# Optimization experiments

Hardware: AMD Instinct MI355X
Metric: run time of the kernel (lower is better)

## Reference

```python
import jax, jax.numpy as jnp
import numpy as np

B, S, D, H = 4, 1024, 1024, 16
DK = D // H
N_REL = 5


def setup_inputs() -> dict:
    key = jax.random.key(0)
    ks = jax.random.split(key, 16)
    p = lambda k, shape: (jax.random.normal(k, shape, dtype=jnp.float32) * 0.02)
    return {
        "x": jax.random.normal(ks[0], (B, S, D), dtype=jnp.float32),
        "relation_matrix": jax.random.randint(ks[1], (S, S), 0, N_REL, dtype=jnp.int32),
        "mask": jax.random.randint(ks[2], (B, 1, S, S), 0, 2, dtype=jnp.int32),
        "Wq": p(ks[3], (D, D)), "bq": p(ks[4], (D,)),
        "Wk": p(ks[5], (D, D)), "bk": p(ks[6], (D,)),
        "Wv": p(ks[7], (D, D)), "bv": p(ks[8], (D,)),
        "Wo": p(ks[9], (D, D)), "bo": p(ks[10], (D,)),
        "rel_table": p(ks[11], (N_REL, DK)),
        "gamma": jnp.ones((D,), dtype=jnp.float32),
        "beta": jnp.zeros((D,), dtype=jnp.float32),
    }


def reference(x, relation_matrix, mask, Wq, bq, Wk, bk, Wv, bv, Wo, bo, rel_table, gamma, beta):
    b, s = x.shape[0], x.shape[1]
    residual = x
    # projections -> [B, H, S, DK]
    def proj(W, bias):
        return (x @ W + bias).reshape(b, s, H, DK).transpose(0, 2, 1, 3)
    Q, K, V = proj(Wq, bq), proj(Wk, bk), proj(Wv, bv)
    scores = jnp.einsum('bhid,bhjd->bhij', Q, K) / jnp.sqrt(jnp.float32(DK))
    # relation-embedding additive bias: gather [S,S,DK] then contract with Q
    rel_emb = rel_table[relation_matrix]               # [S, S, DK]
    rel_scores = jnp.einsum('bhid,ijd->bhij', Q, rel_emb)
    scores = scores + rel_scores * 0.5
    scores = jnp.where(mask == 0, jnp.float32(-1e9), scores)
    attention = jax.nn.softmax(scores, axis=-1)
    context = jnp.einsum('bhij,bhjd->bhid', attention, V)
    context = context.transpose(0, 2, 1, 3).reshape(b, s, D)
    output = context @ Wo + bo
    # layer norm (eps = 1e-5, torch default)
    y = output + residual
    mu = jnp.mean(y, axis=-1, keepdims=True)
    var = jnp.mean(jnp.square(y - mu), axis=-1, keepdims=True)
    return (y - mu) * jax.lax.rsqrt(var + 1e-5) * gamma + beta
```

## Files before the change

### kernel.cpp

```cpp
#include <hip/hip_runtime.h>
#include <hip/hip_bf16.h>

typedef unsigned short u16;
typedef unsigned int u32;
typedef unsigned char u8;
typedef __attribute__((ext_vector_type(8))) short short8;
typedef __attribute__((ext_vector_type(4))) float f32x4;

__device__ __forceinline__ float b2f(u16 u) {
    union { float f; u32 i; } z; z.i = ((u32)u) << 16; return z.f;
}
__device__ __forceinline__ u16 f2b(float f) {
    union { float f; u32 i; } z; z.f = f;
    u32 i = z.i;
    u32 r = (i + 0x7FFFu + ((i >> 16) & 1u)) >> 16;
    return (u16)r;
}
__device__ __forceinline__ float ldf(const void* p, size_t i, int f) {
    return f ? ((const float*)p)[i] : b2f(((const u16*)p)[i]);
}
__device__ __forceinline__ void gload_lds16(const void* g, void* l) {
    __builtin_amdgcn_global_load_lds(
        (const __attribute__((address_space(1))) u32*)g,
        (__attribute__((address_space(3))) u32*)l,
        16, 0, 0);
}

struct P14 { const void* p[14]; };
struct S14 { int s[14]; };

__global__ __launch_bounds__(256) void classify_stats(P14 ptrs, S14 szs, int* stats)
{
    __shared__ int   wsm[4], wzr[4], wag[4], way[4], wjk[4];
    __shared__ float wme[4], wmo[4];
    int i = blockIdx.x;
    int t = threadIdx.x, lane = t & 63, w = t >> 6;
    const u16* p16 = (const u16*)ptrs.p[i];
    const u32* p32 = (const u32*)ptrs.p[i];
    int n = szs.s[i];
    int n16 = n < 4096 ? n : 4096;
    int n32 = n16 >> 1;
    int small = 1, zero = 1, allg = 1, anyg = 0, junk = 0;
    float maxe = 0.f, maxo = 0.f;
    for (int k = t; k < n32; k += 256) if (p32[k] >= 8u) small = 0;
    for (int k = t; k < n16; k += 256) {
        u16 ww = p16[k];
        if (ww != 0) zero = 0;
        if (ww == 0x3F80u) anyg = 1;
        else if (ww != 0) allg = 0;
        float a = fabsf(b2f(ww));
        if (k & 1) { if (a < 1e30f && a > maxo) maxo = a; }
        else { if (!(a < 100.0f)) junk++; else if (a > maxe) maxe = a; }
    }
#pragma unroll
    for (int s = 1; s < 64; s <<= 1) {
        small &= __shfl_xor(small, s);
        zero  &= __shfl_xor(zero, s);
        allg  &= __shfl_xor(allg, s);
        anyg  |= __shfl_xor(anyg, s);
        junk  += __shfl_xor(junk, s);
        maxe   = fmaxf(maxe, __shfl_xor(maxe, s));
        maxo   = fmaxf(maxo, __shfl_xor(maxo, s));
    }
    if (lane == 0) { wsm[w]=small; wzr[w]=zero; wag[w]=allg; way[w]=anyg; wjk[w]=junk; wme[w]=maxe; wmo[w]=maxo; }
    __syncthreads();
    if (t == 0) {
        int sm=1,zr=1,ag=1,ay=0,jk=0; float me=0.f,mo=0.f;
        for (int q=0;q<4;++q){ sm&=wsm[q]; zr&=wzr[q]; ag&=wag[q]; ay|=way[q]; jk+=wjk[q]; me=fmaxf(me,wme[q]); mo=fmaxf(mo,wmo[q]); }
        stats[i*8+0]=sm; stats[i*8+1]=zr; stats[i*8+2]=(ag&&ay)?1:0; stats[i*8+3]=jk;
        stats[i*8+4]=__float_as_int(me); stats[i*8+5]=__float_as_int(mo);
    }
}

__global__ __launch_bounds__(64) void classify_bind(S14 szs, const int* stats, int* cls)
{
    if (threadIdx.x != 0) return;
    int xi = -1, mi = -1, ri = -1, rt = -1, gi = -1, bi = -1;
    int wv[4] = {-1,-1,-1,-1}; int nw = 0;
    int bs[4] = {-1,-1,-1,-1}; int nb = 0;
    for (int i = 0; i < 14; ++i) {
        int s = szs.s[i];
        int sm = stats[i*8+0], zr = stats[i*8+1];
        if (s == 4194304) { if (sm) mi = i; else xi = i; }
        else if (s == 1048576) { if (sm) ri = i; else if (nw < 4) wv[nw++] = i; }
        else if (s == 320) rt = i;
        else if (s == 1024) {
            if (zr) bi = i;
            else if (stats[i*8+2]) gi = i;
            else if (nb < 4) bs[nb++] = i;
        }
    }
    bool ok = (xi >= 0) && (mi >= 0) && (ri >= 0) && (rt >= 0) && (gi >= 0) && (bi >= 0)
           && (nw == 4) && (nb == 4);
    if (ok) {
        cls[0] = xi; cls[1] = ri; cls[2] = mi;
        cls[3] = wv[0]; cls[5] = wv[1]; cls[7] = wv[2]; cls[9] = wv[3];
        cls[4] = bs[0]; cls[6] = bs[1]; cls[8] = bs[2]; cls[10] = bs[3];
        cls[11] = rt; cls[12] = gi; cls[13] = bi;
    } else {
        for (int r = 0; r < 14; ++r) cls[r] = r;
    }
    const int froles[12] = {0,3,4,5,6,7,8,9,10,11,12,13};
    for (int r = 0; r < 12; ++r) {
        int role = froles[r]; int idx = cls[role];
        float me = __int_as_float(stats[idx*8+4]);
        float mo = __int_as_float(stats[idx*8+5]);
        cls[16 + role] = (stats[idx*8+3] > 0) || (me == 0.f && mo > 0.f);
    }
    cls[30] = ok ? 1 : 0;
}

__global__ __launch_bounds__(256) void cvt_x_flex(P14 ptrs, const int* cls, u16* xb) {
    const void* x = ptrs.p[cls[0]];
    int f = cls[16];
    int idx = (blockIdx.x * 256 + threadIdx.x) << 2;
    union { u16 u[4]; uint2 v2; } o;
    if (f) {
        float4 v = *(const float4*)((const float*)x + idx);
        o.u[0] = f2b(v.x); o.u[1] = f2b(v.y); o.u[2] = f2b(v.z); o.u[3] = f2b(v.w);
    } else {
        o.v2 = *(const uint2*)((const u16*)x + idx);
    }
    *(uint2*)&xb[idx] = o.v2;
}

__global__ __launch_bounds__(256) void transposeW_flex(P14 ptrs, const int* cls,
                                                       u16* WT3, u16* WoT)
{
    int z = blockIdx.z;
    const void* W = ptrs.p[cls[3 + 2 * z]];
    int f = cls[16 + 3 + 2 * z];
    u16* WT = (z < 3) ? (WT3 + ((size_t)z << 20)) : WoT;
    __shared__ u16 tile[64][72];
    int t = threadIdx.x;
    int n0 = blockIdx.x << 6, k0 = blockIdx.y << 6;
    int r = t >> 2, c = (t & 3) << 4;
    size_t base = (size_t)(k0 + r) * 1024 + n0 + c;
    if (f) {
        const float* src = (const float*)W + base;
#pragma unroll
        for (int x = 0; x < 16; ++x) tile[r][c + x] = f2b(src[x]);
    } else {
        const u16* src = (const u16*)W + base;
#pragma unroll
        for (int x = 0; x < 16; ++x) tile[r][c + x] = src[x];
    }
    __syncthreads();
    union { u16 u[16]; uint4 v[2]; } tmp;
#pragma unroll
    for (int x = 0; x < 16; ++x) tmp.u[x] = tile[c + x][r];
    *(uint4*)&WT[(size_t)(n0 + r) * 1024 + k0 + c]     = tmp.v[0];
    *(uint4*)&WT[(size_t)(n0 + r) * 1024 + k0 + c + 8] = tmp.v[1];
}

__global__ __launch_bounds__(256) void qrel_k(
    const u16* __restrict__ Q, P14 ptrs, const int* cls, float* __restrict__ Qrel)
{
    __shared__ float rt[5][64];
    const void* rel_table = ptrs.p[cls[11]];
    int f9 = cls[16 + 11];
    int t = threadIdx.x;
    for (int p = t; p < 320; p += 256) ((float*)rt)[p] = ldf(rel_table, p, f9);
    __syncthreads();
    int row = blockIdx.x * 256 + t;
    const u16* qrow = Q + ((size_t)row << 6);
    float a0=0.f, a1=0.f, a2=0.f, a3=0.f, a4=0.f;
#pragma unroll
    for (int k8 = 0; k8 < 64; k8 += 8) {
        union { uint4 v; u16 u[8]; } qq;
        qq.v = *(const uint4*)(qrow + k8);
#pragma unroll
        for (int e = 0; e < 8; ++e) {
            float qv = b2f(qq.u[e]);
            a0 += qv * rt[0][k8 + e];
            a1 += qv * rt[1][k8 + e];
            a2 += qv * rt[2][k8 + e];
            a3 += qv * rt[3][k8 + e];
            a4 += qv * rt[4][k8 + e];
        }
    }
    const float S = 0.5f * 1.44269504f;
    float4 o0 = {a0 * S, a1 * S, a2 * S, a3 * S};
    float4 o1 = {a4 * S, -1e9f, -1e9f, -1e9f};
    *(float4*)&Qrel[(size_t)row * 8]     = o0;
    *(float4*)&Qrel[(size_t)row * 8 + 4] = o1;
}

__global__ __launch_bounds__(256) void gemm128_qkv(
    const u16* __restrict__ X, const u16* __restrict__ WT3,
    P14 ptrs, const int* cls,
    u16* __restrict__ Qb, u16* __restrict__ Kb, u16* __restrict__ VTb)
{
    int o = (blockIdx.x & 7) * 192 + (blockIdx.x >> 3);
    int mt = o / 48, rem = o % 48;
    int z = rem >> 4, nt = rem & 15;
    int m0 = mt << 7, n0 = nt << 6;
    const u16* WT = WT3 + ((size_t)z << 20);
    const void* biasp = ptrs.p[cls[4 + 2 * z]];
    int fb = cls[16 + 4 + 2 * z];
    __shared__ u16 As[2][128][4][8];
    __shared__ u16 Bs[2][64][4][8];
    int t = threadIdx.x, lane = t & 63, w = t >> 6;
    int m = lane & 15, quad = lane >> 4;
    int wm = (w >> 1) << 6, wn = (w & 1) << 5;
    int r1 = t >> 2, r2 = 64 + r1, k4 = t & 3;
    const u16* xa  = &X [(size_t)(m0 + r1) * 1024 + k4 * 8];
    const u16* xa2 = &X [(size_t)(m0 + r2) * 1024 + k4 * 8];
    const u16* wb  = &WT[(size_t)(n0 + r1) * 1024 + k4 * 8];
    f32x4 acc[4][2];
#pragma unroll
    for (int i = 0; i < 4; ++i)
#pragma unroll
        for (int j = 0; j < 2; ++j) acc[i][j] = (f32x4){0.f,0.f,0.f,0.f};

    auto stage = [&](int buf, int k0) {
        gload_lds16(xa  + k0, &As[buf][r1][k4][0]);
        gload_lds16(xa2 + k0, &As[buf][r2][k4][0]);
        gload_lds16(wb  + k0, &Bs[buf][r1][k4][0]);
    };
    stage(0, 0);
    __syncthreads();
    int cur = 0;
    for (int k0 = 0; k0 < 1024; k0 += 32) {
        if (k0 + 32 < 1024) stage(cur ^ 1, k0 + 32);
        short8 af[4], bf[2];
#pragma unroll
        for (int mb = 0; mb < 4; ++mb) af[mb] = *(const short8*)&As[cur][wm + mb*16 + m][quad][0];
#pragma unroll
        for (int nb = 0; nb < 2; ++nb) bf[nb] = *(const short8*)&Bs[cur][wn + nb*16 + m][quad][0];
#pragma unroll
        for (int mb = 0; mb < 4; ++mb)
#pragma unroll
            for (int nb = 0; nb < 2; ++nb)
                acc[mb][nb] = __builtin_amdgcn_mfma_f32_16x16x32_bf16(af[mb], bf[nb], acc[mb][nb], 0, 0, 0);
        __syncthreads();
        cur ^= 1;
    }
    if (z == 2) {
#pragma unroll
        for (int nb = 0; nb < 2; ++nb) {
            int gn = n0 + wn + nb*16 + m;
            int h = gn >> 6, dk = gn & 63;
            float bv = ldf(biasp, gn, fb);
            int sx = (dk & 7) << 3;
#pragma unroll
            for (int mb = 0; mb < 4; ++mb) {
                int gmBase = m0 + wm + mb*16 + (quad << 2);
                int bI = gmBase >> 10, sB = gmBase & 1023;
                int pos = (sB & ~63) | ((sB & 63) ^ sx);
                union { u16 u[4]; uint2 v; } o4;
#pragma unroll
                for (int r = 0; r < 4; ++r) o4.u[r] = f2b(acc[mb][nb][r] + bv);
                *(uint2*)&VTb[((size_t)(bI * 16 + h) << 16) + dk * 1024 + pos] = o4.v;
            }
        }
    } else {
        u16* outp = (z == 0) ? Qb : Kb;
#pragma unroll
        for (int nb = 0; nb < 2; ++nb) {
            int gn = n0 + wn + nb*16 + m;
            int h = gn >> 6, dk = gn & 63;
            float bv = ldf(biasp, gn, fb);
#pragma unroll
            for (int mb = 0; mb < 4; ++mb)
#pragma unroll
                for (int r = 0; r < 4; ++r) {
                    int gm = m0 + wm + mb*16 + (quad << 2) + r;
                    int bI = gm >> 10, s = gm & 1023;
                    int dk2 = (z == 1) ? (dk ^ (((quad * 4 + r) & 7) << 3)) : dk;
                    outp[((size_t)((bI * 16 + h) << 10) + s) * 64 + dk2] = f2b(acc[mb][nb][r] + bv);
                }
        }
    }
}

__global__ __launch_bounds__(256) void gemm_out64(
    const u16* __restrict__ A, const u16* __restrict__ WT,
    P14 ptrs, const int* cls, float* __restrict__ y)
{
    const void* bo   = ptrs.p[cls[10]];
    const void* Xres = ptrs.p[cls[0]];
    int f8 = cls[16 + 10], f0 = cls[16];
    int o = (blockIdx.x & 7) * 128 + (blockIdx.x >> 3);
    int nt = o & 15, mt = o >> 4;
    int n0 = nt << 6, m0 = mt << 6;
    __shared__ u16 As[2][64][4][8];
    __shared__ u16 Bs[2][64][4][8];
    int t = threadIdx.x, lane = t & 63, w = t >> 6;
    int m = lane & 15, quad = lane >> 4;
    int wm = (w >> 1) << 5, wn = (w & 1) << 5;
    int r1 = t >> 2, k4 = t & 3;
    const u16* xa  = &A [(size_t)(m0 + r1) * 1024 + k4 * 8];
    const u16* wb  = &WT[(size_t)(n0 + r1) * 1024 + k4 * 8];
    f32x4 acc[2][2];
#pragma unroll
    for (int i = 0; i < 2; ++i)
#pragma unroll
        for (int j = 0; j < 2; ++j) acc[i][j] = (f32x4){0.f,0.f,0.f,0.f};

    auto stage = [&](int buf, int k0) {
        gload_lds16(xa + k0, &As[buf][r1][k4][0]);
        gload_lds16(wb + k0, &Bs[buf][r1][k4][0]);
    };
    stage(0, 0);
    __syncthreads();
    int cur = 0;
    for (int k0 = 0; k0 < 1024; k0 += 32) {
        if (k0 + 32 < 1024) stage(cur ^ 1, k0 + 32);
        short8 af[2], bf[2];
#pragma unroll
        for (int mb = 0; mb < 2; ++mb) af[mb] = *(const short8*)&As[cur][wm + mb*16 + m][quad][0];
#pragma unroll
        for (int nb = 0; nb < 2; ++nb) bf[nb] = *(const short8*)&Bs[cur][wn + nb*16 + m][quad][0];
#pragma unroll
        for (int mb = 0; mb < 2; ++mb)
#pragma unroll
            for (int nb = 0; nb < 2; ++nb)
                acc[mb][nb] = __builtin_amdgcn_mfma_f32_16x16x32_bf16(af[mb], bf[nb], acc[mb][nb], 0, 0, 0);
        __syncthreads();
        cur ^= 1;
    }
#pragma unroll
    for (int nb = 0; nb < 2; ++nb) {
        int gn = n0 + wn + nb*16 + m;
        float bb = ldf(bo, gn, f8);
#pragma unroll
        for (int mb = 0; mb < 2; ++mb)
#pragma unroll
            for (int r = 0; r < 4; ++r) {
                int gm = m0 + wm + mb*16 + (quad << 2) + r;
                size_t idx = (size_t)gm * 1024 + gn;
                y[idx] = acc[mb][nb][r] + bb + ldf(Xres, idx, f0);
            }
    }
}

__global__ __launch_bounds__(256) void make_codes(P14 ptrs, const int* cls, u8* codes)
{
    const int* relmat = (const int*)ptrs.p[cls[1]];
    const int* maskp  = (const int*)ptrs.p[cls[2]];
    int bid = blockIdx.x;
    int b = bid >> 8, ti = (bid >> 4) & 15, tj = bid & 15;
    int t = threadIdx.x, lane = t & 63, w = t >> 6;
    int m = lane & 15, quad = lane >> 4;
    const int* mb = maskp + ((size_t)b << 20);
    union { uint4 v; u8 c[16]; } out;
#pragma unroll
    for (int jb = 0; jb < 4; ++jb) {
        int j = tj * 64 + jb * 16 + m;
#pragma unroll
        for (int r = 0; r < 4; ++r) {
            int i = ti * 64 + w * 16 + (quad << 2) + r;
            size_t off = (size_t)i * 1024 + j;
            out.c[jb * 4 + r] = mb[off] ? (u8)relmat[off] : (u8)5;
        }
    }
    ((uint4*)codes)[(size_t)bid * 256 + t] = out.v;
}

__global__ __launch_bounds__(256) void attn_mfma(
    const u16* __restrict__ Q, const u16* __restrict__ K, const u16* __restrict__ VT,
    const float* __restrict__ Qrel, const u8* __restrict__ codes, u16* __restrict__ ctx)
{
    int raw = blockIdx.x;
    int bid = (raw & 7) * 128 + (raw >> 3);
    int bh = bid >> 4, ti = bid & 15;
    int i0 = ti << 6;
    int b = bh >> 4, h = bh & 15;
    const u16* Qp = Q  + ((size_t)bh << 16);
    const u16* Kp = K  + ((size_t)bh << 16);
    const u16* Vp = VT + ((size_t)bh << 16);
    const uint4* ctile = (const uint4*)codes + ((size_t)((b * 16 + ti) * 16) << 8);

    __shared__ u16 Ks[2][64][64];
    __shared__ u16 Vt[64][64];
    __shared__ u16 Pls[64][72];
    __shared__ float Qrl[64][9];

    int t = threadIdx.x, lane = t & 63, w = t >> 6;
    int m = lane & 15, quad = lane >> 4;

    {
        float2 qv = *(const float2*)&Qrel[(((size_t)bh << 10) + i0) * 8 + (t << 1)];
        Qrl[t >> 2][(t & 3) << 1]       = qv.x;
        Qrl[t >> 2][((t & 3) << 1) + 1] = qv.y;
    }

    short8 qfrag0, qfrag1;
    {
        const u16* qr = Qp + (size_t)(i0 + w * 16 + m) * 64 + quad * 8;
        qfrag0 = *(const short8*)qr;
        qfrag1 = *(const short8*)(qr + 32);
    }
    f32x4 O[4];
    float l_part[4];
#pragma unroll
    for (int d = 0; d < 4; ++d) O[d] = (f32x4){0.f,0.f,0.f,0.f};
#pragma unroll
    for (int r = 0; r < 4; ++r) l_part[r] = 0.f;

    int srow = t >> 3, scol8 = (t & 7) << 3;
    const u16* ks0 = Kp + (size_t)srow * 64 + scol8;
    const u16* ks1 = ks0 + 32 * 64;
    const u16* vs0 = Vp + (size_t)srow * 1024 + scol8;
    const u16* vs1 = vs0 + 32 * 1024;

    auto stageK = [&](int buf, int j0) {
        gload_lds16(ks0 + (size_t)j0 * 64, &Ks[buf][srow][scol8]);
        gload_lds16(ks1 + (size_t)j0 * 64, &Ks[buf][srow + 32][scol8]);
    };
    auto stageV = [&](int j0) {
        gload_lds16(vs0 + j0, &Vt[srow][scol8]);
        gload_lds16(vs1 + j0, &Vt[srow + 32][scol8]);
    };

    const float SC = 0.125f * 1.44269504f;
    int kx = (m & 7) << 3;

    stageK(0, 0);
    stageV(0);
    uint4 cN = ctile[t];
    __syncthreads();
    int cur = 0;

    for (int j0 = 0; j0 < 1024; j0 += 64) {
        bool next = (j0 + 64 < 1024);
        if (next) stageK(cur ^ 1, j0 + 64);

        f32x4 acc[4];
#pragma unroll
        for (int jb = 0; jb < 4; ++jb) {
            acc[jb] = (f32x4){0.f,0.f,0.f,0.f};
            short8 kb0 = *(const short8*)&Ks[cur][jb * 16 + m][(quad * 8) ^ kx];
            short8 kb1 = *(const short8*)&Ks[cur][jb * 16 + m][(32 + quad * 8) ^ kx];
            acc[jb] = __builtin_amdgcn_mfma_f32_16x16x32_bf16(qfrag0, kb0, acc[jb], 0, 0, 0);
            acc[jb] = __builtin_amdgcn_mfma_f32_16x16x32_bf16(qfrag1, kb1, acc[jb], 0, 0, 0);
        }
        union { uint4 v; u8 c[16]; } cd;
        cd.v = cN;
        if (next) cN = ctile[(((j0 + 64) >> 6) << 8) + t];

        float sc[4][4];
#pragma unroll
        for (int jb = 0; jb < 4; ++jb) {
#pragma unroll
            for (int r = 0; r < 4; ++r) {
                int il = w * 16 + (quad << 2) + r;
                float p = exp2f(acc[jb][r] * SC + Qrl[il][cd.c[jb * 4 + r]]);
                sc[jb][r] = p;
                l_part[r] += p;
            }
        }
#pragma unroll
        for (int jb = 0; jb < 4; ++jb)
#pragma unroll
            for (int r = 0; r < 4; ++r)
                Pls[w * 16 + (quad << 2) + r][jb * 16 + m] = f2b(sc[jb][r]);

        __syncthreads();

        short8 pa0 = *(const short8*)&Pls[w * 16 + m][quad * 8];
        short8 pa1 = *(const short8*)&Pls[w * 16 + m][quad * 8 + 32];
#pragma unroll
        for (int db = 0; db < 4; ++db) {
            short8 vb0 = *(const short8*)&Vt[db * 16 + m][(quad * 8) ^ kx];
            short8 vb1 = *(const short8*)&Vt[db * 16 + m][(32 + quad * 8) ^ kx];
            O[db] = __builtin_amdgcn_mfma_f32_16x16x32_bf16(pa0, vb0, O[db], 0, 0, 0);
            O[db] = __builtin_amdgcn_mfma_f32_16x16x32_bf16(pa1, vb1, O[db], 0, 0, 0);
        }

        __syncthreads();
        if (next) stageV(j0 + 64);
        cur ^= 1;
    }
    float linv[4];
#pragma unroll
    for (int r = 0; r < 4; ++r) {
        float l = l_part[r];
        l += __shfl_xor(l, 1);
        l += __shfl_xor(l, 2);
        l += __shfl_xor(l, 4);
        l += __shfl_xor(l, 8);
        linv[r] = 1.0f / fmaxf(l, 1e-35f);
    }
#pragma unroll
    for (int db = 0; db < 4; ++db)
#pragma unroll
        for (int r = 0; r < 4; ++r) {
            int il = w * 16 + (quad << 2) + r;
            size_t addr = ((size_t)(b * 1024 + i0 + il)) * 1024 + h * 64 + db * 16 + m;
            ctx[addr] = f2b(O[db][r] * linv[r]);
        }
}

__global__ __launch_bounds__(256) void ln_k(
    float* __restrict__ y, P14 ptrs, const int* cls)
{
    const void* gamma = ptrs.p[cls[12]];
    const void* beta  = ptrs.p[cls[13]];
    int f10 = cls[16 + 12], f11 = cls[16 + 13];
    int row = blockIdx.x, t = threadIdx.x;
    float4 v = *(const float4*)&y[(size_t)row * 1024 + (t << 2)];
    float s = v.x + v.y + v.z + v.w;
#pragma unroll
    for (int mm = 1; mm < 64; mm <<= 1) s += __shfl_xor(s, mm);
    __shared__ float sm[8];
    int w = t >> 6, lane = t & 63;
    if (lane == 0) sm[w] = s;
    __syncthreads();
    float mu = (sm[0] + sm[1] + sm[2] + sm[3]) * (1.0f / 1024.0f);
    float dx = v.x - mu, dy = v.y - mu, dz = v.z - mu, dw = v.w - mu;
    float q = dx * dx + dy * dy + dz * dz + dw * dw;
#pragma unroll
    for (int mm = 1; mm < 64; mm <<= 1) q += __shfl_xor(q, mm);
    if (lane == 0) sm[4 + w] = q;
    __syncthreads();
    float var = (sm[4] + sm[5] + sm[6] + sm[7]) * (1.0f / 1024.0f);
    float rs = rsqrtf(var + 1e-5f);
    int c = t << 2;
    float4 o;
    o.x = dx * rs * ldf(gamma, c,     f10) + ldf(beta, c,     f11);
    o.y = dy * rs * ldf(gamma, c + 1, f10) + ldf(beta, c + 1, f11);
    o.z = dz * rs * ldf(gamma, c + 2, f10) + ldf(beta, c + 2, f11);
    o.w = dw * rs * ldf(gamma, c + 3, f10) + ldf(beta, c + 3, f11);
    *(float4*)&y[(size_t)row * 1024 + c] = o;
}

extern "C" void kernel_launch(void* const* d_in, const int* in_sizes, int n_in,
                              void* d_out, int out_size, void* d_ws, size_t ws_size,
                              hipStream_t stream) {
    (void)out_size; (void)ws_size;
    P14 ptrs; S14 szs;
    for (int i = 0; i < 14; ++i) {
        ptrs.p[i] = (i < n_in) ? d_in[i] : d_in[0];
        szs.s[i]  = (i < n_in) ? in_sizes[i] : 0;
    }
    float* out = (float*)d_out;

    char* ws = (char*)d_ws;
    const size_t MB = 1u << 20;
    u16*   WT3   = (u16*)(ws);
    u16*   WoT   = (u16*)(ws + 6 * MB);
    u16*   Xb    = (u16*)(ws + 8 * MB);
    u16*   Qb    = (u16*)(ws + 16 * MB);
    u16*   Kb    = (u16*)(ws + 24 * MB);
    u16*   VTb   = (u16*)(ws + 32 * MB);
    u16*   ctx   = (u16*)(ws + 8 * MB);
    u8*    codes = (u8*)(ws);
    float* Qrel  = (float*)(ws + 4 * MB);
    int*   cls   = (int*)(ws + 40 * MB);
    int*   stats = (int*)(ws + 40 * MB + 512);

    classify_stats<<<14, 256, 0, stream>>>(ptrs, szs, stats);
    classify_bind<<<1, 64, 0, stream>>>(szs, stats, cls);
    cvt_x_flex<<<4096, 256, 0, stream>>>(ptrs, cls, Xb);
    transposeW_flex<<<dim3(16, 16, 4), 256, 0, stream>>>(ptrs, cls, WT3, WoT);
    gemm128_qkv<<<1536, 256, 0, stream>>>(Xb, WT3, ptrs, cls, Qb, Kb, VTb);
    qrel_k<<<256, 256, 0, stream>>>(Qb, ptrs, cls, Qrel);
    make_codes<<<1024, 256, 0, stream>>>(ptrs, cls, codes);
    attn_mfma<<<1024, 256, 0, stream>>>(Qb, Kb, VTb, Qrel, codes, ctx);
    gemm_out64<<<1024, 256, 0, stream>>>(ctx, WoT, ptrs, cls, out);
    ln_k<<<4096, 256, 0, stream>>>(out, ptrs, cls);
}
```

Before: 284.8 us.

## Fuse Q, K, V projections into one GEMM block sharing the X tile

Each block now computes the Q, K and V output tiles for the same 128-row X tile, loading X into shared memory once and reusing its fragments across all three weight matrices. This cuts X global/LDS traffic by a factor of three and reduces the grid from 1536 to 512 blocks. In exchange, accumulator registers triple (96 floats per thread) and LDS use grows, which may lower occupancy. With 512 blocks on the device's CUs, fewer waves are available to hide latency.

```diff
diff --git a/kernel.cpp b/kernel.cpp
--- a/kernel.cpp
+++ b/kernel.cpp
@@ -186,90 +186,101 @@
     *(float4*)&Qrel[(size_t)row * 8 + 4] = o1;
 }
 
-__global__ __launch_bounds__(256) void gemm128_qkv(
+__global__ __launch_bounds__(256) void gemm_qkv_fused(
     const u16* __restrict__ X, const u16* __restrict__ WT3,
     P14 ptrs, const int* cls,
     u16* __restrict__ Qb, u16* __restrict__ Kb, u16* __restrict__ VTb)
 {
-    int o = (blockIdx.x & 7) * 192 + (blockIdx.x >> 3);
-    int mt = o / 48, rem = o % 48;
-    int z = rem >> 4, nt = rem & 15;
+    int o = (blockIdx.x & 7) * 64 + (blockIdx.x >> 3);
+    int mt = o >> 4, nt = o & 15;
     int m0 = mt << 7, n0 = nt << 6;
-    const u16* WT = WT3 + ((size_t)z << 20);
-    const void* biasp = ptrs.p[cls[4 + 2 * z]];
-    int fb = cls[16 + 4 + 2 * z];
     __shared__ u16 As[2][128][4][8];
-    __shared__ u16 Bs[2][64][4][8];
+    __shared__ u16 Bs[3][2][64][4][8];
     int t = threadIdx.x, lane = t & 63, w = t >> 6;
     int m = lane & 15, quad = lane >> 4;
     int wm = (w >> 1) << 6, wn = (w & 1) << 5;
     int r1 = t >> 2, r2 = 64 + r1, k4 = t & 3;
-    const u16* xa  = &X [(size_t)(m0 + r1) * 1024 + k4 * 8];
-    const u16* xa2 = &X [(size_t)(m0 + r2) * 1024 + k4 * 8];
-    const u16* wb  = &WT[(size_t)(n0 + r1) * 1024 + k4 * 8];
-    f32x4 acc[4][2];
-#pragma unroll
-    for (int i = 0; i < 4; ++i)
-#pragma unroll
-        for (int j = 0; j < 2; ++j) acc[i][j] = (f32x4){0.f,0.f,0.f,0.f};
+    const u16* xa  = &X  [(size_t)(m0 + r1) * 1024 + k4 * 8];
+    const u16* xa2 = &X  [(size_t)(m0 + r2) * 1024 + k4 * 8];
+    const u16* wb0 = &WT3[(size_t)(n0 + r1) * 1024 + k4 * 8];
+    const u16* wb1 = wb0 + (1u << 20);
+    const u16* wb2 = wb0 + (2u << 20);
+    f32x4 acc[3][4][2];
+#pragma unroll
+    for (int z = 0; z < 3; ++z)
+#pragma unroll
+        for (int i = 0; i < 4; ++i)
+#pragma unroll
+            for (int j = 0; j < 2; ++j) acc[z][i][j] = (f32x4){0.f,0.f,0.f,0.f};
 
     auto stage = [&](int buf, int k0) {
         gload_lds16(xa  + k0, &As[buf][r1][k4][0]);
         gload_lds16(xa2 + k0, &As[buf][r2][k4][0]);
-        gload_lds16(wb  + k0, &Bs[buf][r1][k4][0]);
+        gload_lds16(wb0 + k0, &Bs[0][buf][r1][k4][0]);
+        gload_lds16(wb1 + k0, &Bs[1][buf][r1][k4][0]);
+        gload_lds16(wb2 + k0, &Bs[2][buf][r1][k4][0]);
     };
     stage(0, 0);
     __syncthreads();
     int cur = 0;
     for (int k0 = 0; k0 < 1024; k0 += 32) {
         if (k0 + 32 < 1024) stage(cur ^ 1, k0 + 32);
-        short8 af[4], bf[2];
+        short8 af[4];
 #pragma unroll
         for (int mb = 0; mb < 4; ++mb) af[mb] = *(const short8*)&As[cur][wm + mb*16 + m][quad][0];
 #pragma unroll
-        for (int nb = 0; nb < 2; ++nb) bf[nb] = *(const short8*)&Bs[cur][wn + nb*16 + m][quad][0];
-#pragma unroll
-        for (int mb = 0; mb < 4; ++mb)
-#pragma unroll
-            for (int nb = 0; nb < 2; ++nb)
-                acc[mb][nb] = __builtin_amdgcn_mfma_f32_16x16x32_bf16(af[mb], bf[nb], acc[mb][nb], 0, 0, 0);
+        for (int z = 0; z < 3; ++z) {
+            short8 bf0 = *(const short8*)&Bs[z][cur][wn + m][quad][0];
+            short8 bf1 = *(const short8*)&Bs[z][cur][wn + 16 + m][quad][0];
+#pragma unroll
+            for (int mb = 0; mb < 4; ++mb) {
+                acc[z][mb][0] = __builtin_amdgcn_mfma_f32_16x16x32_bf16(af[mb], bf0, acc[z][mb][0], 0, 0, 0);
+                acc[z][mb][1] = __builtin_amdgcn_mfma_f32_16x16x32_bf16(af[mb], bf1, acc[z][mb][1], 0, 0, 0);
+            }
+        }
         __syncthreads();
         cur ^= 1;
     }
-    if (z == 2) {
-#pragma unroll
-        for (int nb = 0; nb < 2; ++nb) {
-            int gn = n0 + wn + nb*16 + m;
-            int h = gn >> 6, dk = gn & 63;
-            float bv = ldf(biasp, gn, fb);
-            int sx = (dk & 7) << 3;
-#pragma unroll
-            for (int mb = 0; mb < 4; ++mb) {
-                int gmBase = m0 + wm + mb*16 + (quad << 2);
-                int bI = gmBase >> 10, sB = gmBase & 1023;
-                int pos = (sB & ~63) | ((sB & 63) ^ sx);
-                union { u16 u[4]; uint2 v; } o4;
-#pragma unroll
-                for (int r = 0; r < 4; ++r) o4.u[r] = f2b(acc[mb][nb][r] + bv);
-                *(uint2*)&VTb[((size_t)(bI * 16 + h) << 16) + dk * 1024 + pos] = o4.v;
+#pragma unroll
+    for (int z = 0; z < 3; ++z) {
+        const void* biasp = ptrs.p[cls[4 + 2 * z]];
+        int fb = cls[16 + 4 + 2 * z];
+        if (z == 2) {
+#pragma unroll
+            for (int nb = 0; nb < 2; ++nb) {
+                int gn = n0 + wn + nb*16 + m;
+                int h = gn >> 6, dk = gn & 63;
+                float bv = ldf(biasp, gn, fb);
+                int sx = (dk & 7) << 3;
+#pragma unroll
+                for (int mb = 0; mb < 4; ++mb) {
+                    int gmBase = m0 + wm + mb*16 + (quad << 2);
+                    int bI = gmBase >> 10, sB = gmBase & 1023;
+                    int pos = (sB & ~63) | ((sB & 63) ^ sx);
+                    union { u16 u[4]; uint2 v; } o4;
+#pragma unroll
+                    for (int r = 0; r < 4; ++r) o4.u[r] = f2b(acc[2][mb][nb][r] + bv);
+                    *(uint2*)&VTb[((size_t)(bI * 16 + h) << 16) + dk * 1024 + pos] = o4.v;
+                }
             }
-        }
-    } else {
-        u16* outp = (z == 0) ? Qb : Kb;
-#pragma unroll
-        for (int nb = 0; nb < 2; ++nb) {
-            int gn = n0 + wn + nb*16 + m;
-            int h = gn >> 6, dk = gn & 63;
-            float bv = ldf(biasp, gn, fb);
-#pragma unroll
-            for (int mb = 0; mb < 4; ++mb)
-#pragma unroll
-                for (int r = 0; r < 4; ++r) {
-                    int gm = m0 + wm + mb*16 + (quad << 2) + r;
-                    int bI = gm >> 10, s = gm & 1023;
-                    int dk2 = (z == 1) ? (dk ^ (((quad * 4 + r) & 7) << 3)) : dk;
-                    outp[((size_t)((bI * 16 + h) << 10) + s) * 64 + dk2] = f2b(acc[mb][nb][r] + bv);
-                }
+        } else {
+            u16* outp = (z == 0) ? Qb : Kb;
+#pragma unroll
+            for (int nb = 0; nb < 2; ++nb) {
+                int gn = n0 + wn + nb*16 + m;
+                int h = gn >> 6, dk = gn & 63;
+                float bv = ldf(biasp, gn, fb);
+#pragma unroll
+                for (int mb = 0; mb < 4; ++mb)
+#pragma unroll
+                    for (int r = 0; r < 4; ++r) {
+                        int gm = m0 + wm + mb*16 + (quad << 2) + r;
+                        int bI = gm >> 10, s = gm & 1023;
+                        int dk2 = (z == 1) ? (dk ^ (((quad * 4 + r) & 7) << 3)) : dk;
+                        outp[((size_t)((bI * 16 + h) << 10) + s) * 64 + dk2] =
+                            f2b(acc[z][mb][nb][r] + bv);
+                    }
+            }
         }
     }
 }
@@ -555,7 +566,7 @@
     classify_bind<<<1, 64, 0, stream>>>(szs, stats, cls);
     cvt_x_flex<<<4096, 256, 0, stream>>>(ptrs, cls, Xb);
     transposeW_flex<<<dim3(16, 16, 4), 256, 0, stream>>>(ptrs, cls, WT3, WoT);
-    gemm128_qkv<<<1536, 256, 0, stream>>>(Xb, WT3, ptrs, cls, Qb, Kb, VTb);
+    gemm_qkv_fused<<<512, 256, 0, stream>>>(Xb, WT3, ptrs, cls, Qb, Kb, VTb);
     qrel_k<<<256, 256, 0, stream>>>(Qb, ptrs, cls, Qrel);
     make_codes<<<1024, 256, 0, stream>>>(ptrs, cls, codes);
     attn_mfma<<<1024, 256, 0, stream>>>(Qb, Kb, VTb, Qrel, codes, ctx);
```

Result: slower. 291.8 us (+2.4%).

## Deepen GEMM LDS prefetch so two k-tiles stay in flight

Applied to the files above, without the earlier changes.

Both the QKV projection GEMM and the output projection GEMM now issue loads for the first two k-tiles before the loop. Each later tile's async global-to-LDS load is issued right after the compute barrier. Partial vmcnt waits let the next tile's load stay outstanding while the current tile is consumed, replacing the full __syncthreads drain. This aims to hide global memory latency behind the MFMA work. In exchange it adds a second barrier per iteration and depends on hand-counted vmcnt values being correct.

```diff
diff --git a/kernel.cpp b/kernel.cpp
--- a/kernel.cpp
+++ b/kernel.cpp
@@ -219,10 +219,12 @@
         gload_lds16(wb  + k0, &Bs[buf][r1][k4][0]);
     };
     stage(0, 0);
-    __syncthreads();
+    stage(1, 32);
+    asm volatile("s_waitcnt vmcnt(3)" ::: "memory");
+    __builtin_amdgcn_s_barrier();
+    __builtin_amdgcn_sched_barrier(0);
     int cur = 0;
     for (int k0 = 0; k0 < 1024; k0 += 32) {
-        if (k0 + 32 < 1024) stage(cur ^ 1, k0 + 32);
         short8 af[4], bf[2];
 #pragma unroll
         for (int mb = 0; mb < 4; ++mb) af[mb] = *(const short8*)&As[cur][wm + mb*16 + m][quad][0];
@@ -233,7 +235,16 @@
 #pragma unroll
             for (int nb = 0; nb < 2; ++nb)
                 acc[mb][nb] = __builtin_amdgcn_mfma_f32_16x16x32_bf16(af[mb], bf[nb], acc[mb][nb], 0, 0, 0);
-        __syncthreads();
+        __builtin_amdgcn_s_barrier();
+        __builtin_amdgcn_sched_barrier(0);
+        if (k0 + 64 < 1024) {
+            stage(cur, k0 + 64);
+            asm volatile("s_waitcnt vmcnt(3)" ::: "memory");
+        } else {
+            asm volatile("s_waitcnt vmcnt(0)" ::: "memory");
+        }
+        __builtin_amdgcn_s_barrier();
+        __builtin_amdgcn_sched_barrier(0);
         cur ^= 1;
     }
     if (z == 2) {
@@ -303,10 +314,12 @@
         gload_lds16(wb + k0, &Bs[buf][r1][k4][0]);
     };
     stage(0, 0);
-    __syncthreads();
+    stage(1, 32);
+    asm volatile("s_waitcnt vmcnt(2)" ::: "memory");
+    __builtin_amdgcn_s_barrier();
+    __builtin_amdgcn_sched_barrier(0);
     int cur = 0;
     for (int k0 = 0; k0 < 1024; k0 += 32) {
-        if (k0 + 32 < 1024) stage(cur ^ 1, k0 + 32);
         short8 af[2], bf[2];
 #pragma unroll
         for (int mb = 0; mb < 2; ++mb) af[mb] = *(const short8*)&As[cur][wm + mb*16 + m][quad][0];
@@ -317,7 +330,16 @@
 #pragma unroll
             for (int nb = 0; nb < 2; ++nb)
                 acc[mb][nb] = __builtin_amdgcn_mfma_f32_16x16x32_bf16(af[mb], bf[nb], acc[mb][nb], 0, 0, 0);
-        __syncthreads();
+        __builtin_amdgcn_s_barrier();
+        __builtin_amdgcn_sched_barrier(0);
+        if (k0 + 64 < 1024) {
+            stage(cur, k0 + 64);
+            asm volatile("s_waitcnt vmcnt(2)" ::: "memory");
+        } else {
+            asm volatile("s_waitcnt vmcnt(0)" ::: "memory");
+        }
+        __builtin_amdgcn_s_barrier();
+        __builtin_amdgcn_sched_barrier(0);
         cur ^= 1;
     }
 #pragma unroll
```

Result: faster. 276.1 us (-3.1%).
